# Kernel tuning notes

Measured on AMD Instinct MI355X. Metric: run time of the kernel, lower is better.

## Reference

```python
import jax, jax.numpy as jnp
import numpy as np

HIDDEN = 128

def setup_inputs() -> dict:
    key = jax.random.key(0)
    ks = jax.random.split(key, 7)
    B, T, I, O = 256, 512, 256, 1000
    s_ih = 1.0 / np.sqrt(HIDDEN)
    x = jax.random.normal(ks[0], (B, T, I), dtype=jnp.float32)
    W_ih = jax.random.uniform(ks[1], (HIDDEN, I), minval=-s_ih, maxval=s_ih, dtype=jnp.float32)
    W_hh = jax.random.uniform(ks[2], (HIDDEN, HIDDEN), minval=-s_ih, maxval=s_ih, dtype=jnp.float32)
    b_ih = jax.random.uniform(ks[3], (HIDDEN,), minval=-s_ih, maxval=s_ih, dtype=jnp.float32)
    b_hh = jax.random.uniform(ks[4], (HIDDEN,), minval=-s_ih, maxval=s_ih, dtype=jnp.float32)
    s_fc = 1.0 / np.sqrt(HIDDEN)
    W_fc = jax.random.uniform(ks[5], (O, HIDDEN), minval=-s_fc, maxval=s_fc, dtype=jnp.float32)
    b_fc = jax.random.uniform(ks[6], (O,), minval=-s_fc, maxval=s_fc, dtype=jnp.float32)
    return {"x": x, "W_ih": W_ih, "W_hh": W_hh, "b_ih": b_ih, "b_hh": b_hh, "W_fc": W_fc, "b_fc": b_fc}


def reference(x, W_ih, W_hh, b_ih, b_hh, W_fc, b_fc):
    B = x.shape[0]
    # Precompute input projection for all timesteps in one big GEMM: [B,T,H]
    xp = jnp.einsum('bti,hi->bth', x, W_ih) + b_ih + b_hh
    h0 = jnp.zeros((B, HIDDEN), dtype=x.dtype)

    def step(h, xp_t):
        h = jnp.tanh(xp_t + h @ W_hh.T)
        return h, None

    # scan over time axis; only the final hidden state feeds the fc head
    h_last, _ = jax.lax.scan(step, h0, jnp.swapaxes(xp, 0, 1))
    return h_last @ W_fc.T + b_fc
```

## Files before the change

### kernel.cpp

```cpp
#include <hip/hip_runtime.h>


#define HID    128
#define TSTEPS 512
#define BATCH  256
#define INDIM  256
#define ODIM   1000

typedef _Float16 f16x8 __attribute__((ext_vector_type(8)));
typedef __fp16   fp16x2 __attribute__((ext_vector_type(2)));
typedef float    f32x4 __attribute__((ext_vector_type(4)));

__device__ __forceinline__ unsigned pk16(float a, float b) {
    union { fp16x2 h; unsigned u; } t;
    t.h = __builtin_amdgcn_cvt_pkrtz(a, b);
    return t.u;
}
__device__ __forceinline__ float tanh_fast(float v) {
    float e = __expf(2.f * v);
    float r = __builtin_amdgcn_rcpf(e + 1.f);
    return __builtin_fmaf(-2.f, r, 1.f);
}

__global__ __launch_bounds__(256) void k_phase1(const float* __restrict__ x,
                                                const float* __restrict__ Wih,
                                                const float* __restrict__ bih,
                                                const float* __restrict__ bhh,
                                                float* __restrict__ xp) {
    __shared__ __align__(16) _Float16 xs[2][4096];
    __shared__ __align__(16) _Float16 wsm[2][4096];

    const int tid  = threadIdx.x;
    const int wave = tid >> 6, lane = tid & 63;
    const int quad = lane >> 4, l16 = lane & 15;
    const int wm = wave >> 1, wn = wave & 1;
    const int m0 = blockIdx.x * 128;

    int srow[4], scol[4], sdst[4];
#pragma unroll
    for (int q = 0; q < 4; q++) {
        int li = q * 256 + tid;
        srow[q] = li >> 3;
        scol[q] = li & 7;
        sdst[q] = srow[q] * 32 + ((((scol[q] >> 1) ^ srow[q]) & 3) << 3) + ((scol[q] & 1) << 2);
    }

    float bias_v[4];
#pragma unroll
    for (int nt = 0; nt < 4; nt++) {
        int j = wn * 64 + nt * 16 + l16;
        bias_v[nt] = bih[j] + bhh[j];
    }

    float4 rx[4], rw[4];
#define LOAD_STAGE(KC)                                                              \
    {                                                                               \
        _Pragma("unroll") for (int q = 0; q < 4; q++) {                             \
            rx[q] = *(const float4*)(x + (size_t)(m0 + srow[q]) * INDIM + (KC) * 32 + scol[q] * 4); \
            rw[q] = *(const float4*)(Wih + (size_t)srow[q] * INDIM + (KC) * 32 + scol[q] * 4);      \
        }                                                                           \
    }
#define WRITE_STAGE(BUF)                                                            \
    {                                                                               \
        _Pragma("unroll") for (int q = 0; q < 4; q++) {                             \
            uint2 px, pw;                                                           \
            px.x = pk16(rx[q].x, rx[q].y); px.y = pk16(rx[q].z, rx[q].w);           \
            pw.x = pk16(rw[q].x, rw[q].y); pw.y = pk16(rw[q].z, rw[q].w);           \
            *(uint2*)&xs[BUF][sdst[q]]  = px;                                       \
            *(uint2*)&wsm[BUF][sdst[q]] = pw;                                       \
        }                                                                           \
    }

    f32x4 acc[4][4];
#pragma unroll
    for (int mt = 0; mt < 4; mt++)
#pragma unroll
        for (int nt = 0; nt < 4; nt++) {
            acc[mt][nt].x = 0.f; acc[mt][nt].y = 0.f;
            acc[mt][nt].z = 0.f; acc[mt][nt].w = 0.f;
        }

    LOAD_STAGE(0);
    WRITE_STAGE(0);
    __syncthreads();

    for (int kc = 0; kc < 8; kc++) {
        const int b = kc & 1;
        if (kc < 7) LOAD_STAGE(kc + 1);

        f16x8 a[4], bw[4];
#pragma unroll
        for (int mt = 0; mt < 4; mt++) {
            int row = wm * 64 + mt * 16 + l16;
            a[mt] = *(const f16x8*)&xs[b][row * 32 + (((quad ^ row) & 3) << 3)];
        }
#pragma unroll
        for (int nt = 0; nt < 4; nt++) {
            int row = wn * 64 + nt * 16 + l16;
            bw[nt] = *(const f16x8*)&wsm[b][row * 32 + (((quad ^ row) & 3) << 3)];
        }
#pragma unroll
        for (int mt = 0; mt < 4; mt++)
#pragma unroll
            for (int nt = 0; nt < 4; nt++)
                acc[mt][nt] = __builtin_amdgcn_mfma_f32_16x16x32_f16(a[mt], bw[nt], acc[mt][nt], 0, 0, 0);

        if (kc < 7) WRITE_STAGE(b ^ 1);
        __syncthreads();
    }

#pragma unroll
    for (int mt = 0; mt < 4; mt++)
#pragma unroll
        for (int nt = 0; nt < 4; nt++)
#pragma unroll
            for (int reg = 0; reg < 4; reg++) {
                int row = m0 + wm * 64 + mt * 16 + quad * 4 + reg;
                xp[(size_t)row * HID + wn * 64 + nt * 16 + l16] = acc[mt][nt][reg] + bias_v[nt];
            }
#undef LOAD_STAGE
#undef WRITE_STAGE
}

#define RNN_STEP4(TV, XQI, XQC, PB) {                                             \
    _Pragma("unroll") for (int reg = 0; reg < 4; reg++) {                         \
        float hv = tanh_fast(C[reg]);                                             \
        int m = quad * 4 + reg;                                                   \
        hp[PB][m * 128 + ((((jbase >> 3) ^ m) & 15) << 3) + (jbase & 7)] =        \
            (_Float16)hv;                                                         \
    }                                                                             \
    if ((TV) + 4 < TSTEPS) {                                                      \
        _Pragma("unroll") for (int reg = 0; reg < 4; reg++)                       \
            XQI[reg] = xpb[ib[reg] + ((TV) + 4) * HID];                           \
    }                                                                             \
    __syncthreads();                                                              \
    f16x8 A[4];                                                                   \
    _Pragma("unroll") for (int kc = 0; kc < 4; kc++)                              \
        A[kc] = *(const f16x8*)&hp[PB][l16 * 128 + ((((kc * 4 + quad) ^ l16) & 15) << 3)]; \
    f32x4 ch, cl;                                                                 \
    ch.x = XQC[0]; ch.y = XQC[1]; ch.z = XQC[2]; ch.w = XQC[3];                   \
    cl.x = 0.f; cl.y = 0.f; cl.z = 0.f; cl.w = 0.f;                               \
    ch = __builtin_amdgcn_mfma_f32_16x16x32_f16(A[0], Bf[0], ch, 0, 0, 0);        \
    cl = __builtin_amdgcn_mfma_f32_16x16x32_f16(A[2], Bf[2], cl, 0, 0, 0);        \
    ch = __builtin_amdgcn_mfma_f32_16x16x32_f16(A[1], Bf[1], ch, 0, 0, 0);        \
    cl = __builtin_amdgcn_mfma_f32_16x16x32_f16(A[3], Bf[3], cl, 0, 0, 0);        \
    C = ch + cl;                                                                  \
}

__global__ __launch_bounds__(512) void k_rnn4(const float* __restrict__ Whh,
                                              float* __restrict__ ws) {
    __shared__ __align__(16) _Float16 hp[2][16 * 128];
    const int tid  = threadIdx.x;
    const int wave = tid >> 6, lane = tid & 63;
    const int quad = lane >> 4, l16 = lane & 15;
    const int r0    = blockIdx.x * 16;
    const int jbase = wave * 16 + l16;

    f16x8 Bf[4];
#pragma unroll
    for (int kc = 0; kc < 4; kc++) {
        const float* p = Whh + (size_t)jbase * HID + kc * 32 + quad * 8;
        float4 e0 = *(const float4*)p, e1 = *(const float4*)(p + 4);
        union { unsigned u[4]; f16x8 v; } t;
        t.u[0] = pk16(e0.x, e0.y); t.u[1] = pk16(e0.z, e0.w);
        t.u[2] = pk16(e1.x, e1.y); t.u[3] = pk16(e1.z, e1.w);
        Bf[kc] = t.v;
    }

    const float* xpb = ws;
    int ib[4];
#pragma unroll
    for (int reg = 0; reg < 4; reg++)
        ib[reg] = (r0 + quad * 4 + reg) * (TSTEPS * HID) + jbase;

    f32x4 C;
    float xq0[4], xq1[4], xq2[4], xq3[4];
    C.x = xpb[ib[0]]; C.y = xpb[ib[1]]; C.z = xpb[ib[2]]; C.w = xpb[ib[3]];
#pragma unroll
    for (int reg = 0; reg < 4; reg++) {
        xq1[reg] = xpb[ib[reg] + 1 * HID];
        xq2[reg] = xpb[ib[reg] + 2 * HID];
        xq3[reg] = xpb[ib[reg] + 3 * HID];
    }

    for (int t = 0; t < 508; t += 4) {
        RNN_STEP4(t,     xq0, xq1, 0);
        RNN_STEP4(t + 1, xq1, xq2, 1);
        RNN_STEP4(t + 2, xq2, xq3, 0);
        RNN_STEP4(t + 3, xq3, xq0, 1);
    }
    RNN_STEP4(508, xq0, xq1, 0);
    RNN_STEP4(509, xq1, xq2, 1);
    RNN_STEP4(510, xq2, xq3, 0);

#pragma unroll
    for (int reg = 0; reg < 4; reg++)
        ws[ib[reg]] = tanh_fast(C[reg]);
}

__global__ __launch_bounds__(256) void k_fc(const float* __restrict__ ws,
                                            const float* __restrict__ Wfc,
                                            const float* __restrict__ bfc,
                                            float* __restrict__ out) {
    __shared__ float hb[HID];
    const int b   = blockIdx.x;
    const int tid = threadIdx.x;
    if (tid < HID) hb[tid] = ws[(size_t)b * (TSTEPS * HID) + tid];
    __syncthreads();

    for (int o = tid; o < ODIM; o += 256) {
        const float* wr = Wfc + (size_t)o * HID;
        float acc = 0.f;
#pragma unroll
        for (int q = 0; q < 32; q++) {
            float4 wv = *(const float4*)(wr + q * 4);
            float4 hv = *(const float4*)&hb[q * 4];
            acc += wv.x * hv.x + wv.y * hv.y + wv.z * hv.z + wv.w * hv.w;
        }
        out[(size_t)b * ODIM + o] = acc + bfc[o];
    }
}

extern "C" void kernel_launch(void* const* d_in, const int* in_sizes, int n_in,
                              void* d_out, int out_size, void* d_ws, size_t ws_size,
                              hipStream_t stream) {
    const float* x   = (const float*)d_in[0];
    const float* Wih = (const float*)d_in[1];
    const float* Whh = (const float*)d_in[2];
    const float* bih = (const float*)d_in[3];
    const float* bhh = (const float*)d_in[4];
    const float* Wfc = (const float*)d_in[5];
    const float* bfc = (const float*)d_in[6];
    float* out = (float*)d_out;
    float* ws  = (float*)d_ws;

    k_phase1<<<dim3(1024), dim3(256), 0, stream>>>(x, Wih, bih, bhh, ws);
    k_rnn4  <<<dim3(16),   dim3(512), 0, stream>>>(Whh, ws);
    k_fc    <<<dim3(BATCH), dim3(256), 0, stream>>>(ws, Wfc, bfc, out);
}
```

Measured before the change: 393.0 us.

## Transpose RNN MFMA so W_hh is A operand, halve waves per block

Rewrites the recurrent kernel so each wave computes a 32-column hidden slice for 16 batch rows. W_hh is held in registers as the MFMA A operand and the hidden state is read from LDS as the B operand. The block shrinks from 8 to 4 waves, which makes each per-step __syncthreads cheaper. Each lane now gets packed fp16 LDS stores and float4 loads of the precomputed input, replacing scalar ones. In exchange, each wave runs a serial chain of 4 MFMAs per tile instead of two split accumulators, which lengthens per-step latency.

Measured after the change: 409.0 us. 4.1% more time.

```diff
diff --git a/kernel.cpp b/kernel.cpp
--- a/kernel.cpp
+++ b/kernel.cpp
@@ -122,80 +122,97 @@
 #undef WRITE_STAGE
 }
 
-#define RNN_STEP4(TV, XQI, XQC, PB) {                                             \
-    _Pragma("unroll") for (int reg = 0; reg < 4; reg++) {                         \
-        float hv = tanh_fast(C[reg]);                                             \
-        int m = quad * 4 + reg;                                                   \
-        hp[PB][m * 128 + ((((jbase >> 3) ^ m) & 15) << 3) + (jbase & 7)] =        \
-            (_Float16)hv;                                                         \
+#define RNN_STEP5(TV, XQI, XQC, PB) {                                             \
+    {                                                                             \
+        float h0 = tanh_fast(C[0][0]), h1 = tanh_fast(C[0][1]);                   \
+        float h2 = tanh_fast(C[0][2]), h3 = tanh_fast(C[0][3]);                   \
+        uint2 pw; pw.x = pk16(h0, h1); pw.y = pk16(h2, h3);                       \
+        *(uint2*)&hp[PB][wadr0] = pw;                                             \
+        h0 = tanh_fast(C[1][0]); h1 = tanh_fast(C[1][1]);                         \
+        h2 = tanh_fast(C[1][2]); h3 = tanh_fast(C[1][3]);                         \
+        pw.x = pk16(h0, h1); pw.y = pk16(h2, h3);                                 \
+        *(uint2*)&hp[PB][wadr1] = pw;                                             \
     }                                                                             \
     if ((TV) + 4 < TSTEPS) {                                                      \
-        _Pragma("unroll") for (int reg = 0; reg < 4; reg++)                       \
-            XQI[reg] = xpb[ib[reg] + ((TV) + 4) * HID];                           \
+        XQI[0] = *(const float4*)(xb + ((TV) + 4) * HID);                         \
+        XQI[1] = *(const float4*)(xb + ((TV) + 4) * HID + 16);                    \
     }                                                                             \
     __syncthreads();                                                              \
-    f16x8 A[4];                                                                   \
+    f16x8 Bv[4];                                                                  \
     _Pragma("unroll") for (int kc = 0; kc < 4; kc++)                              \
-        A[kc] = *(const f16x8*)&hp[PB][l16 * 128 + ((((kc * 4 + quad) ^ l16) & 15) << 3)]; \
-    f32x4 ch, cl;                                                                 \
-    ch.x = XQC[0]; ch.y = XQC[1]; ch.z = XQC[2]; ch.w = XQC[3];                   \
-    cl.x = 0.f; cl.y = 0.f; cl.z = 0.f; cl.w = 0.f;                               \
-    ch = __builtin_amdgcn_mfma_f32_16x16x32_f16(A[0], Bf[0], ch, 0, 0, 0);        \
-    cl = __builtin_amdgcn_mfma_f32_16x16x32_f16(A[2], Bf[2], cl, 0, 0, 0);        \
-    ch = __builtin_amdgcn_mfma_f32_16x16x32_f16(A[1], Bf[1], ch, 0, 0, 0);        \
-    cl = __builtin_amdgcn_mfma_f32_16x16x32_f16(A[3], Bf[3], cl, 0, 0, 0);        \
-    C = ch + cl;                                                                  \
-}
-
-__global__ __launch_bounds__(512) void k_rnn4(const float* __restrict__ Whh,
+        Bv[kc] = *(const f16x8*)&hp[PB][radr[kc]];                                \
+    _Pragma("unroll") for (int jt = 0; jt < 2; jt++) {                            \
+        f32x4 c;                                                                  \
+        c.x = XQC[jt].x; c.y = XQC[jt].y; c.z = XQC[jt].z; c.w = XQC[jt].w;       \
+        c = __builtin_amdgcn_mfma_f32_16x16x32_f16(Af[jt][0], Bv[0], c, 0, 0, 0); \
+        c = __builtin_amdgcn_mfma_f32_16x16x32_f16(Af[jt][1], Bv[1], c, 0, 0, 0); \
+        c = __builtin_amdgcn_mfma_f32_16x16x32_f16(Af[jt][2], Bv[2], c, 0, 0, 0); \
+        c = __builtin_amdgcn_mfma_f32_16x16x32_f16(Af[jt][3], Bv[3], c, 0, 0, 0); \
+        C[jt] = c;                                                                \
+    }                                                                             \
+}
+
+__global__ __launch_bounds__(256) void k_rnn5(const float* __restrict__ Whh,
                                               float* __restrict__ ws) {
     __shared__ __align__(16) _Float16 hp[2][16 * 128];
     const int tid  = threadIdx.x;
     const int wave = tid >> 6, lane = tid & 63;
     const int quad = lane >> 4, l16 = lane & 15;
-    const int r0    = blockIdx.x * 16;
-    const int jbase = wave * 16 + l16;
-
-    f16x8 Bf[4];
-#pragma unroll
-    for (int kc = 0; kc < 4; kc++) {
-        const float* p = Whh + (size_t)jbase * HID + kc * 32 + quad * 8;
-        float4 e0 = *(const float4*)p, e1 = *(const float4*)(p + 4);
-        union { unsigned u[4]; f16x8 v; } t;
-        t.u[0] = pk16(e0.x, e0.y); t.u[1] = pk16(e0.z, e0.w);
-        t.u[2] = pk16(e1.x, e1.y); t.u[3] = pk16(e1.z, e1.w);
-        Bf[kc] = t.v;
-    }
-
-    const float* xpb = ws;
-    int ib[4];
-#pragma unroll
-    for (int reg = 0; reg < 4; reg++)
-        ib[reg] = (r0 + quad * 4 + reg) * (TSTEPS * HID) + jbase;
-
-    f32x4 C;
-    float xq0[4], xq1[4], xq2[4], xq3[4];
-    C.x = xpb[ib[0]]; C.y = xpb[ib[1]]; C.z = xpb[ib[2]]; C.w = xpb[ib[3]];
-#pragma unroll
-    for (int reg = 0; reg < 4; reg++) {
-        xq1[reg] = xpb[ib[reg] + 1 * HID];
-        xq2[reg] = xpb[ib[reg] + 2 * HID];
-        xq3[reg] = xpb[ib[reg] + 3 * HID];
-    }
+    const int r0   = blockIdx.x * 16;
+    const int jb0  = wave * 32;
+
+    f16x8 Af[2][4];
+#pragma unroll
+    for (int jt = 0; jt < 2; jt++)
+#pragma unroll
+        for (int kc = 0; kc < 4; kc++) {
+            const float* p = Whh + (size_t)(jb0 + jt * 16 + l16) * HID + kc * 32 + quad * 8;
+            float4 e0 = *(const float4*)p, e1 = *(const float4*)(p + 4);
+            union { unsigned u[4]; f16x8 v; } t;
+            t.u[0] = pk16(e0.x, e0.y); t.u[1] = pk16(e0.z, e0.w);
+            t.u[2] = pk16(e1.x, e1.y); t.u[3] = pk16(e1.z, e1.w);
+            Af[jt][kc] = t.v;
+        }
+
+    const int jg0 = jb0 + quad * 4;
+    const int jg1 = jb0 + 16 + quad * 4;
+    const int wadr0 = l16 * 128 + ((((jg0 >> 3) ^ l16) & 15) << 3) + (jg0 & 7);
+    const int wadr1 = l16 * 128 + ((((jg1 >> 3) ^ l16) & 15) << 3) + (jg1 & 7);
+    int radr[4];
+#pragma unroll
+    for (int kc = 0; kc < 4; kc++)
+        radr[kc] = l16 * 128 + ((((kc * 4 + quad) ^ l16) & 15) << 3);
+
+    const float* xb = ws + (size_t)(r0 + l16) * (TSTEPS * HID) + jb0 + quad * 4;
+
+    f32x4 C[2];
+    float4 Q0[2], Q1[2], Q2[2], Q3[2];
+    {
+        float4 a = *(const float4*)(xb);
+        float4 b = *(const float4*)(xb + 16);
+        C[0].x = a.x; C[0].y = a.y; C[0].z = a.z; C[0].w = a.w;
+        C[1].x = b.x; C[1].y = b.y; C[1].z = b.z; C[1].w = b.w;
+    }
+    Q1[0] = *(const float4*)(xb + 1 * HID); Q1[1] = *(const float4*)(xb + 1 * HID + 16);
+    Q2[0] = *(const float4*)(xb + 2 * HID); Q2[1] = *(const float4*)(xb + 2 * HID + 16);
+    Q3[0] = *(const float4*)(xb + 3 * HID); Q3[1] = *(const float4*)(xb + 3 * HID + 16);
 
     for (int t = 0; t < 508; t += 4) {
-        RNN_STEP4(t,     xq0, xq1, 0);
-        RNN_STEP4(t + 1, xq1, xq2, 1);
-        RNN_STEP4(t + 2, xq2, xq3, 0);
-        RNN_STEP4(t + 3, xq3, xq0, 1);
-    }
-    RNN_STEP4(508, xq0, xq1, 0);
-    RNN_STEP4(509, xq1, xq2, 1);
-    RNN_STEP4(510, xq2, xq3, 0);
-
-#pragma unroll
-    for (int reg = 0; reg < 4; reg++)
-        ws[ib[reg]] = tanh_fast(C[reg]);
+        RNN_STEP5(t,     Q0, Q1, 0);
+        RNN_STEP5(t + 1, Q1, Q2, 1);
+        RNN_STEP5(t + 2, Q2, Q3, 0);
+        RNN_STEP5(t + 3, Q3, Q0, 1);
+    }
+    RNN_STEP5(508, Q0, Q1, 0);
+    RNN_STEP5(509, Q1, Q2, 1);
+    RNN_STEP5(510, Q2, Q3, 0);
+
+#pragma unroll
+    for (int jt = 0; jt < 2; jt++)
+#pragma unroll
+        for (int reg = 0; reg < 4; reg++)
+            ws[(size_t)(r0 + l16) * (TSTEPS * HID) + jb0 + jt * 16 + quad * 4 + reg] =
+                tanh_fast(C[jt][reg]);
 }
 
 __global__ __launch_bounds__(256) void k_fc(const float* __restrict__ ws,
@@ -235,6 +252,6 @@
     float* ws  = (float*)d_ws;
 
     k_phase1<<<dim3(1024), dim3(256), 0, stream>>>(x, Wih, bih, bhh, ws);
-    k_rnn4  <<<dim3(16),   dim3(512), 0, stream>>>(Whh, ws);
+    k_rnn5  <<<dim3(16),   dim3(256), 0, stream>>>(Whh, ws);
     k_fc    <<<dim3(BATCH), dim3(256), 0, stream>>>(ws, Wfc, bfc, out);
 }
```
